# Kernel optimization log

Hardware: AMD Instinct MI355X
Metric: run time of the kernel (lower is better)

Reference implementation:

```python
import jax, jax.numpy as jnp
import numpy as np

NI = 512
HEADS = 8
DH = NI // HEADS  # 64 = attn_chans
EPS = 1e-5

def _ln(x, g, b):
    mu = jnp.mean(x, axis=-1, keepdims=True)
    var = jnp.var(x, axis=-1, keepdims=True)
    return (x - mu) * jax.lax.rsqrt(var + EPS) * g + b

def setup_inputs() -> dict:
    key = jax.random.key(0)
    ks = jax.random.split(key, 5)
    n, c, h, w = 8, NI, 32, 32
    return {
        "x": jax.random.normal(ks[0], (n, c, h, w), jnp.float32),
        "query_x": jax.random.normal(ks[1], (n, c, h, w), jnp.float32),
        "q_ln_g": jnp.ones((c,), jnp.float32),
        "q_ln_b": jnp.zeros((c,), jnp.float32),
        "q_w": jax.random.normal(ks[2], (c, c), jnp.float32) / np.sqrt(c),
        "q_b": jnp.zeros((c,), jnp.float32),
        "kv_ln_g": jnp.ones((c,), jnp.float32),
        "kv_ln_b": jnp.zeros((c,), jnp.float32),
        "kv_w": jax.random.normal(ks[3], (c, 2 * c), jnp.float32) / np.sqrt(c),
        "kv_b": jnp.zeros((2 * c,), jnp.float32),
        "proj_w": jax.random.normal(ks[4], (c, c), jnp.float32) / np.sqrt(c),
        "proj_b": jnp.zeros((c,), jnp.float32),
    }

def reference(x, query_x, q_ln_g, q_ln_b, q_w, q_b, kv_ln_g, kv_ln_b, kv_w, kv_b, proj_w, proj_b):
    n, c, h, w = x.shape
    s = h * w
    xs = x.reshape(n, c, s).transpose(0, 2, 1)        # (n, s, c)
    qx = query_x.reshape(n, c, s).transpose(0, 2, 1)  # (n, s, c)
    q_proj = _ln(qx, q_ln_g, q_ln_b) @ q_w + q_b        # (n, s, c)
    kv = _ln(xs, kv_ln_g, kv_ln_b) @ kv_w + kv_b        # (n, s, 2c)
    cat = jnp.concatenate([q_proj, kv], axis=-1)        # (n, s, 3c)
    # rearrange 'n s (h d3)' with h=HEADS, d3 = 3*DH, then chunk into q,k,v
    cat = cat.reshape(n, s, HEADS, 3 * DH).transpose(0, 2, 1, 3)  # (n, H, s, 3d)
    q, k, v = jnp.split(cat, 3, axis=-1)                # each (n, H, s, d)
    scale = jnp.sqrt(jnp.asarray(DH, q.dtype))          # sqrt(ni/nheads)
    scores = jnp.einsum('nhqd,nhkd->nhqk', q, k) / scale
    attn = jax.nn.softmax(scores, axis=-1)
    o = jnp.einsum('nhqk,nhkd->nhqd', attn, v)          # (n, H, s, d)
    o = o.transpose(0, 2, 1, 3).reshape(n, s, c)        # (n, s, c)
    o = o @ proj_w + proj_b
    return o.transpose(0, 2, 1).reshape(n, c, h, w)
```

## Files before the change

### kernel.cpp

```cpp
#include <hip/hip_runtime.h>
#include <math.h>

namespace {

constexpr int S = 1024;
constexpr int C = 512;
constexpr int NBATCH = 8;
constexpr int RTOT = NBATCH * S;
constexpr int HEADS = 8;
constexpr int DH = 64;

typedef __attribute__((ext_vector_type(8))) short bf16x8;
typedef __attribute__((ext_vector_type(4))) float f32x4;
typedef __attribute__((ext_vector_type(16))) float f32x16;
typedef unsigned short u16;
typedef unsigned int u32;

__device__ __forceinline__ u16 f2bf(float x) {
  union { float f; u32 u; } v; v.f = x;
  u32 r = v.u + 0x7FFF + ((v.u >> 16) & 1);
  return (u16)(r >> 16);
}
__device__ __forceinline__ float bf2f(u16 b) {
  union { u32 u; float f; } v; v.u = (u32)b << 16; return v.f;
}
__device__ __forceinline__ u32 cvtpk(float a, float b) {
  u32 r;
  asm("v_cvt_pk_bf16_f32 %0, %1, %2" : "=v"(r) : "v"(a), "v"(b));
  return r;
}
__device__ __forceinline__ float fexp2(float x) {
  float r;
  asm("v_exp_f32 %0, %1" : "=v"(r) : "v"(x));
  return r;
}
__device__ __forceinline__ void gl_lds16(const void* g, void* l) {
  auto gp = (const __attribute__((address_space(1))) u32*)g;
  auto lp = (__attribute__((address_space(3))) u32*)l;
  __builtin_amdgcn_global_load_lds(gp, lp, 16, 0, 0);
}

__global__ void ln_fused(const float* __restrict__ x, const float* __restrict__ qx,
                         const float* __restrict__ gx, const float* __restrict__ bx,
                         const float* __restrict__ gq, const float* __restrict__ bq,
                         u16* __restrict__ Xkv, u16* __restrict__ Xq) {
  __shared__ float Ssum[8][32], Ssq[8][32];
  __shared__ float mu_s[32], rs_s[32];
  __shared__ float T[32][65];
  int t = threadIdx.x;
  int si0 = blockIdx.x * 32;
  int isq = blockIdx.y & 1, n = blockIdx.y >> 1;
  const float* in = isq ? qx : x;
  const float* g  = isq ? gq : gx;
  const float* be = isq ? bq : bx;
  u16* out = isq ? Xq : Xkv;

  {
    int sl = t & 31, cg = t >> 5;
    const float* p = in + ((size_t)n * C + cg * 64) * S + si0 + sl;
    float s = 0.f, sq = 0.f;
#pragma unroll 8
    for (int c = 0; c < 64; c++) { float v = p[(size_t)c * S]; s += v; sq += v * v; }
    Ssum[cg][sl] = s; Ssq[cg][sl] = sq;
  }
  __syncthreads();
  if (t < 32) {
    float ss = 0.f, q2 = 0.f;
#pragma unroll
    for (int i = 0; i < 8; i++) { ss += Ssum[i][t]; q2 += Ssq[i][t]; }
    float m = ss * (1.0f / C);
    float var = q2 * (1.0f / C) - m * m;
    mu_s[t] = m; rs_s[t] = rsqrtf(var + 1e-5f);
  }
  __syncthreads();

  int si4 = (t & 7) * 4, cl = t >> 3;
  float4 mu4 = *(const float4*)&mu_s[si4];
  float4 rs4 = *(const float4*)&rs_s[si4];
  int wsl = t >> 3, wc8 = (t & 7) * 8;

  for (int c0 = 0; c0 < C; c0 += 64) {
#pragma unroll
    for (int i = 0; i < 2; i++) {
      int c = c0 + cl + i * 32;
      float4 v = *(const float4*)&in[((size_t)n * C + c) * S + si0 + si4];
      float gg = g[c], bb = be[c];
      T[si4 + 0][cl + i * 32] = (v.x - mu4.x) * rs4.x * gg + bb;
      T[si4 + 1][cl + i * 32] = (v.y - mu4.y) * rs4.y * gg + bb;
      T[si4 + 2][cl + i * 32] = (v.z - mu4.z) * rs4.z * gg + bb;
      T[si4 + 3][cl + i * 32] = (v.w - mu4.w) * rs4.w * gg + bb;
    }
    __syncthreads();
    u16 pk[8];
#pragma unroll
    for (int j = 0; j < 8; j++) pk[j] = f2bf(T[wsl][wc8 + j]);
    *(uint4*)&out[((size_t)(n * S + si0 + wsl)) * C + c0 + wc8] = *(const uint4*)pk;
    __syncthreads();
  }
}

__global__ void prep_w(const float* __restrict__ qw, const float* __restrict__ kvw,
                       const float* __restrict__ pw,
                       u16* __restrict__ Wtq, u16* __restrict__ Wtkv,
                       u16* __restrict__ Wph) {
  int z = blockIdx.z;
  int N = (z == 1) ? 1024 : 512;
  int col0 = blockIdx.y * 64;
  if (col0 >= N) return;
  int k0 = blockIdx.x * 64;
  const float* W = (z == 0) ? qw : (z == 1) ? kvw : pw;
  __shared__ float T[64][65];
  int t = threadIdx.x;
  int kl = t >> 4, c4 = (t & 15) * 4;
#pragma unroll
  for (int i = 0; i < 4; i++) {
    float4 v = *(const float4*)&W[(size_t)(k0 + kl + i * 16) * N + col0 + c4];
    T[kl + i * 16][c4 + 0] = v.x; T[kl + i * 16][c4 + 1] = v.y;
    T[kl + i * 16][c4 + 2] = v.z; T[kl + i * 16][c4 + 3] = v.w;
  }
  __syncthreads();
#pragma unroll
  for (int p = 0; p < 2; p++) {
    int cl = (t >> 3) + p * 32, k8 = (t & 7) * 8;
    u16 hi[8];
#pragma unroll
    for (int j = 0; j < 8; j++) hi[j] = f2bf(T[k8 + j][cl]);
    size_t o = (size_t)(col0 + cl) * 512 + k0 + k8;
    if (z == 0) *(uint4*)&Wtq[o] = *(const uint4*)hi;
    else if (z == 1) *(uint4*)&Wtkv[o] = *(const uint4*)hi;
    else *(uint4*)&Wph[o] = *(const uint4*)hi;
  }
}

__global__ __launch_bounds__(256, 4) void gemm_qkv(
    const u16* __restrict__ Xq, const u16* __restrict__ Xkv,
    const u16* __restrict__ Wtq, const u16* __restrict__ Wtkv,
    const float* __restrict__ q_b, const float* __restrict__ kv_b,
    u16* __restrict__ Qb, u16* __restrict__ Kb, u16* __restrict__ Vt) {
  __shared__ __attribute__((aligned(16))) u16 As[128 * 64];
  __shared__ __attribute__((aligned(16))) u16 Bs[128 * 64];
  int t = threadIdx.x, wid = t >> 6, lane = t & 63, lr = lane & 15, lg = lane >> 4;
  int colb = blockIdx.x;
  const u16* A; const u16* Wt; const float* bias; int ch0;
  if (colb < 4) { A = Xq;  Wt = Wtq  + (size_t)colb * 128 * 512;       bias = q_b  + colb * 128;       ch0 = colb * 128; }
  else          { A = Xkv; Wt = Wtkv + (size_t)(colb - 4) * 128 * 512; bias = kv_b + (colb - 4) * 128; ch0 = 512 + (colb - 4) * 128; }
  int row0 = blockIdx.y * 128;
  int wr = wid >> 1, wc = wid & 1;
  f32x4 acc[4][4];
#pragma unroll
  for (int m = 0; m < 4; m++)
#pragma unroll
    for (int n = 0; n < 4; n++) acc[m][n] = (f32x4){0.f, 0.f, 0.f, 0.f};

  for (int k0 = 0; k0 < 512; k0 += 64) {
    __syncthreads();
#pragma unroll
    for (int it = 0; it < 4; it++) {
      int chunk = (wid * 4 + it) * 64 + lane;
      int r = chunk >> 3, sg = chunk & 7;
      gl_lds16(A + (size_t)(row0 + r) * 512 + k0 + ((sg ^ (r & 7)) * 8),
               (char*)As + (size_t)chunk * 16);
    }
#pragma unroll
    for (int it = 0; it < 4; it++) {
      int chunk = (wid * 4 + it) * 64 + lane;
      int r = chunk >> 3, sg = chunk & 7;
      gl_lds16(Wt + (size_t)r * 512 + k0 + ((sg ^ (r & 7)) * 8),
               (char*)Bs + (size_t)chunk * 16);
    }
    __syncthreads();
#pragma unroll
    for (int kk = 0; kk < 2; kk++) {
      bf16x8 bfr[4];
#pragma unroll
      for (int n = 0; n < 4; n++) {
        int col = wc * 64 + n * 16 + lr;
        bfr[n] = *(const bf16x8*)((const char*)Bs + col * 128 + (((kk * 4 + lg) ^ (col & 7)) << 4));
      }
#pragma unroll
      for (int m = 0; m < 4; m++) {
        int row = wr * 64 + m * 16 + lr;
        bf16x8 af = *(const bf16x8*)((const char*)As + row * 128 + (((kk * 4 + lg) ^ (row & 7)) << 4));
#pragma unroll
        for (int n = 0; n < 4; n++)
          acc[m][n] = __builtin_amdgcn_mfma_f32_16x16x32_bf16(af, bfr[n], acc[m][n], 0, 0, 0);
      }
    }
  }
#pragma unroll
  for (int m = 0; m < 4; m++)
#pragma unroll
    for (int n = 0; n < 4; n++) {
      int colg = wc * 64 + n * 16 + lr;
      int ch = ch0 + colg;
      int h = ch / 192, role = (ch >> 6) % 3, d = ch & 63;
      float bs = bias[colg];
      float qsc = (role == 0) ? 0.18033688f : 1.0f;
      int growb = row0 + wr * 64 + m * 16 + lg * 4;
      int nn = growb >> 10, ssi0 = growb & (S - 1);
      size_t nh = (size_t)(nn * HEADS + h);
      if (role == 2) {
        u16 pk[4];
#pragma unroll
        for (int r = 0; r < 4; r++) pk[r] = f2bf(acc[m][n][r] + bs);
        *(uint2*)&Vt[(nh * DH + d) * S + ssi0] = *(const uint2*)pk;
      } else {
        u16* dst = (role == 0) ? Qb : Kb;
#pragma unroll
        for (int r = 0; r < 4; r++)
          dst[(nh * S + ssi0 + r) * DH + d] = f2bf((acc[m][n][r] + bs) * qsc);
      }
    }
}

__global__ __launch_bounds__(256) void gemm_proj(
    const u16* __restrict__ Aob, const u16* __restrict__ Wh,
    const float* __restrict__ bias, float* __restrict__ out) {
  __shared__ __attribute__((aligned(16))) u16 As[128 * 64];
  __shared__ __attribute__((aligned(16))) u16 Bh[64 * 64];
  int t = threadIdx.x, wid = t >> 6, lane = t & 63, lr = lane & 15, lg = lane >> 4;
  int ch0 = blockIdx.x * 64, row0 = blockIdx.y * 128;
  int wc = wid & 1, wr = wid >> 1;
  f32x4 acc[2][4];
#pragma unroll
  for (int m = 0; m < 2; m++)
#pragma unroll
    for (int n = 0; n < 4; n++) acc[m][n] = (f32x4){0.f, 0.f, 0.f, 0.f};

  for (int k0 = 0; k0 < 512; k0 += 64) {
    __syncthreads();
#pragma unroll
    for (int it = 0; it < 4; it++) {
      int idx = (wid * 4 + it) * 64 + lane;
      int r = idx >> 3, sg = idx & 7;
      gl_lds16(Aob + (size_t)(row0 + r) * 512 + k0 + ((sg ^ (r & 7)) * 8),
               (char*)As + (wid * 4 + it) * 1024);
    }
#pragma unroll
    for (int it = 0; it < 2; it++) {
      int idx = (wid * 2 + it) * 64 + lane;
      int r = idx >> 3, sg = idx & 7;
      gl_lds16(Wh + (size_t)(ch0 + r) * 512 + k0 + ((sg ^ (r & 7)) * 8),
               (char*)Bh + (wid * 2 + it) * 1024);
    }
    __syncthreads();
#pragma unroll
    for (int kk = 0; kk < 2; kk++) {
      bf16x8 ar[4];
#pragma unroll
      for (int n = 0; n < 4; n++) {
        int row = wr * 64 + n * 16 + lr;
        ar[n] = *(const bf16x8*)((const char*)As + row * 128 + (((kk * 4 + lg) ^ (row & 7)) << 4));
      }
#pragma unroll
      for (int m = 0; m < 2; m++) {
        int ch = wc * 32 + m * 16 + lr;
        bf16x8 bh = *(const bf16x8*)((const char*)Bh + ch * 128 + (((kk * 4 + lg) ^ (ch & 7)) << 4));
#pragma unroll
        for (int n = 0; n < 4; n++)
          acc[m][n] = __builtin_amdgcn_mfma_f32_16x16x32_bf16(bh, ar[n], acc[m][n], 0, 0, 0);
      }
    }
  }
#pragma unroll
  for (int m = 0; m < 2; m++)
#pragma unroll
    for (int n = 0; n < 4; n++) {
      int rowg = row0 + wr * 64 + n * 16 + lr;
      int nn = rowg >> 10, ssi = rowg & (S - 1);
#pragma unroll
      for (int r = 0; r < 4; r++) {
        int ch = ch0 + wc * 32 + m * 16 + lg * 4 + r;
        out[((size_t)nn * C + ch) * S + ssi] = acc[m][n][r] + bias[ch];
      }
    }
}

constexpr int KVB = 64;

__global__ __launch_bounds__(256, 4) void attn_kernel(
    const u16* __restrict__ Qbf, const u16* __restrict__ Kbf,
    const u16* __restrict__ Vtb, u16* __restrict__ Obf) {
  __shared__ __attribute__((aligned(16))) u16 Ks[2][KVB * DH];
  __shared__ __attribute__((aligned(16))) u16 Vs[2][DH * KVB];

  int tid = threadIdx.x;
  int wave = tid >> 6, lane = tid & 63;
  int lq = lane & 31, hi = lane >> 5;
  int qg = wave & 1, kg = wave >> 1;
  int w = (blockIdx.x & 7) * 128 + (blockIdx.x >> 3);
  int qt = w & 15, nh = w >> 4;
  const u16* Qg = Qbf + (size_t)nh * S * DH;
  const u16* Kg = Kbf + (size_t)nh * S * DH;
  const u16* Vg = Vtb + (size_t)nh * DH * S;

  int qrow = qt * 64 + qg * 32 + lq;
  bf16x8 qf[4];
#pragma unroll
  for (int ks = 0; ks < 4; ks++)
    qf[ks] = *(const bf16x8*)(Qg + (size_t)qrow * DH + ks * 16 + hi * 8);

  f32x16 oa0 = {}, oa1 = {};
  float m_run = -1e30f, l_run = 0.f;

  int e0i = tid, e1i = tid + 256;
  int r0 = e0i >> 3, sg0 = e0i & 7, r1 = e1i >> 3, sg1 = e1i & 7;
  char* kd0 = (char*)&Ks[0][0] + (e0i & ~63) * 16;
  char* kd1 = (char*)&Ks[0][0] + (e1i & ~63) * 16;
  char* vd0 = (char*)&Vs[0][0] + (e0i & ~63) * 16;
  char* vd1 = (char*)&Vs[0][0] + (e1i & ~63) * 16;

#define STAGE(kb, b)                                                             \
  do {                                                                           \
    gl_lds16(Kg + (size_t)((kb) * KVB + r0) * 64 + ((sg0 ^ (r0 & 7)) * 8),       \
             kd0 + (b) * (KVB * DH * 2));                                        \
    gl_lds16(Kg + (size_t)((kb) * KVB + r1) * 64 + ((sg1 ^ (r1 & 7)) * 8),       \
             kd1 + (b) * (KVB * DH * 2));                                        \
    gl_lds16(Vg + (size_t)r0 * S + (kb) * KVB + ((sg0 ^ (r0 & 7)) * 8),          \
             vd0 + (b) * (KVB * DH * 2));                                        \
    gl_lds16(Vg + (size_t)r1 * S + (kb) * KVB + ((sg1 ^ (r1 & 7)) * 8),          \
             vd1 + (b) * (KVB * DH * 2));                                        \
  } while (0)

  STAGE(0, 0);

  for (int kb = 0; kb < S / KVB; kb++) {
    int cur = kb & 1;
    __syncthreads();
    if (kb + 1 < S / KVB) STAGE(kb + 1, cur ^ 1);

    const char* Kc = (const char*)&Ks[cur][0];
    const char* Vc = (const char*)&Vs[cur][0];

    f32x16 sc = {};
#pragma unroll
    for (int ks = 0; ks < 4; ks++) {
      int sg = ks * 2 + hi;
      bf16x8 kf = *(const bf16x8*)(Kc + (kg * 32 + lq) * 128 + ((sg ^ (lq & 7)) << 4));
      sc = __builtin_amdgcn_mfma_f32_32x32x16_bf16(kf, qf[ks], sc, 0, 0, 0);
    }

    bf16x8 vfr[2][2];
#pragma unroll
    for (int kk = 0; kk < 2; kk++) {
      int sg = kg * 4 + kk * 2 + hi;
      vfr[kk][0] = *(const bf16x8*)(Vc + lq * 128 + ((sg ^ (lq & 7)) << 4));
      vfr[kk][1] = *(const bf16x8*)(Vc + (32 + lq) * 128 + ((sg ^ (lq & 7)) << 4));
    }

    float mx[8];
#pragma unroll
    for (int r = 0; r < 8; r++) mx[r] = fmaxf(sc[2 * r], sc[2 * r + 1]);
#pragma unroll
    for (int r = 0; r < 4; r++) mx[r] = fmaxf(mx[r], mx[r + 4]);
    float pmax = fmaxf(fmaxf(mx[0], mx[1]), fmaxf(mx[2], mx[3]));
    pmax = fmaxf(pmax, __shfl_xor(pmax, 32));

    if (!__all(pmax <= m_run + 11.5f)) {
      float mnew = fmaxf(m_run, pmax);
      float corr = fexp2(m_run - mnew);
      m_run = mnew;
      l_run *= corr;
#pragma unroll
      for (int r = 0; r < 16; r++) { oa0[r] *= corr; oa1[r] *= corr; }
    }

#pragma unroll
    for (int r = 0; r < 16; r++) sc[r] = fexp2(sc[r] - m_run);
    {
      float s8[8];
#pragma unroll
      for (int r = 0; r < 8; r++) s8[r] = sc[2 * r] + sc[2 * r + 1];
#pragma unroll
      for (int r = 0; r < 4; r++) s8[r] += s8[r + 4];
      float psum = (s8[0] + s8[1]) + (s8[2] + s8[3]);
      psum += __shfl_xor(psum, 32);
      l_run += psum;
    }

    u32 c[8];
    c[0] = cvtpk(sc[0],  sc[1]);  c[1] = cvtpk(sc[2],  sc[3]);
    c[2] = cvtpk(sc[4],  sc[5]);  c[3] = cvtpk(sc[6],  sc[7]);
    c[4] = cvtpk(sc[8],  sc[9]);  c[5] = cvtpk(sc[10], sc[11]);
    c[6] = cvtpk(sc[12], sc[13]); c[7] = cvtpk(sc[14], sc[15]);
    asm("v_permlane32_swap_b32 %0, %1" : "+v"(c[0]), "+v"(c[2]));
    asm("v_permlane32_swap_b32 %0, %1" : "+v"(c[1]), "+v"(c[3]));
    asm("v_permlane32_swap_b32 %0, %1" : "+v"(c[4]), "+v"(c[6]));
    asm("v_permlane32_swap_b32 %0, %1" : "+v"(c[5]), "+v"(c[7]));

#pragma unroll
    for (int kk = 0; kk < 2; kk++) {
      union { u32 u[4]; bf16x8 v; } pu;
      pu.u[0] = c[kk * 4 + 0]; pu.u[1] = c[kk * 4 + 1];
      pu.u[2] = c[kk * 4 + 2]; pu.u[3] = c[kk * 4 + 3];
      oa0 = __builtin_amdgcn_mfma_f32_32x32x16_bf16(vfr[kk][0], pu.v, oa0, 0, 0, 0);
      oa1 = __builtin_amdgcn_mfma_f32_32x32x16_bf16(vfr[kk][1], pu.v, oa1, 0, 0, 0);
    }
  }
#undef STAGE

  __syncthreads();
  float* exO = (float*)&Ks[0][0];
  float* exS = (float*)&Vs[0][0];
  if (kg) {
    float* o = exO + qg * 2048;
#pragma unroll
    for (int r = 0; r < 16; r++) {
      o[r * 64 + lane] = oa0[r];
      o[(16 + r) * 64 + lane] = oa1[r];
    }
    exS[qg * 128 + lane] = m_run;
    exS[qg * 128 + 64 + lane] = l_run;
  }
  __syncthreads();
  if (!kg) {
    float* o = exO + qg * 2048;
    float m2 = exS[qg * 128 + lane];
    float l2 = exS[qg * 128 + 64 + lane];
    float m = fmaxf(m_run, m2);
    float f0 = fexp2(m_run - m), f2 = fexp2(m2 - m);
    l_run = l_run * f0 + l2 * f2;
#pragma unroll
    for (int r = 0; r < 16; r++) {
      oa0[r] = oa0[r] * f0 + o[r * 64 + lane] * f2;
      oa1[r] = oa1[r] * f0 + o[(16 + r) * 64 + lane] * f2;
    }
    int n = nh >> 3, h = nh & 7;
    float lf = 1.0f / l_run;
    u16* orow = Obf + ((size_t)n * S + qrow) * C + h * DH;
#pragma unroll
    for (int rq = 0; rq < 4; rq++) {
      int d0 = rq * 8 + 4 * hi;
      uint2 w0, w1;
      w0.x = cvtpk(oa0[rq * 4 + 0] * lf, oa0[rq * 4 + 1] * lf);
      w0.y = cvtpk(oa0[rq * 4 + 2] * lf, oa0[rq * 4 + 3] * lf);
      w1.x = cvtpk(oa1[rq * 4 + 0] * lf, oa1[rq * 4 + 1] * lf);
      w1.y = cvtpk(oa1[rq * 4 + 2] * lf, oa1[rq * 4 + 3] * lf);
      *(uint2*)(orow + d0) = w0;
      *(uint2*)(orow + 32 + d0) = w1;
    }
  }
}

}

extern "C" void kernel_launch(void* const* d_in, const int* in_sizes, int n_in,
                              void* d_out, int out_size, void* d_ws, size_t ws_size,
                              hipStream_t stream) {
  const float* x       = (const float*)d_in[0];
  const float* qx      = (const float*)d_in[1];
  const float* q_ln_g  = (const float*)d_in[2];
  const float* q_ln_b  = (const float*)d_in[3];
  const float* q_w     = (const float*)d_in[4];
  const float* q_b     = (const float*)d_in[5];
  const float* kv_ln_g = (const float*)d_in[6];
  const float* kv_ln_b = (const float*)d_in[7];
  const float* kv_w    = (const float*)d_in[8];
  const float* kv_b    = (const float*)d_in[9];
  const float* proj_w  = (const float*)d_in[10];
  const float* proj_b  = (const float*)d_in[11];
  float* out = (float*)d_out;

  u16* u = (u16*)d_ws;
  u16* Xkv  = u;                u += (size_t)RTOT * C;
  u16* Xq   = u;                u += (size_t)RTOT * C;
  u16* Wtq  = u;                u += (size_t)C * C;
  u16* Wtkv = u;                u += (size_t)2 * C * C;
  u16* Wph  = u;                u += (size_t)C * C;
  u16* Qb   = u;                u += (size_t)NBATCH * HEADS * S * DH;
  u16* Kb   = u;                u += (size_t)NBATCH * HEADS * S * DH;
  u16* Vt   = u;                u += (size_t)NBATCH * HEADS * S * DH;
  u16* Obf  = u;

  hipLaunchKernelGGL(ln_fused, dim3(S / 32, 2 * NBATCH), dim3(256), 0, stream,
                     x, qx, kv_ln_g, kv_ln_b, q_ln_g, q_ln_b, Xkv, Xq);
  hipLaunchKernelGGL(prep_w, dim3(8, 16, 3), dim3(256), 0, stream,
                     q_w, kv_w, proj_w, Wtq, Wtkv, Wph);
  hipLaunchKernelGGL(gemm_qkv, dim3(12, RTOT / 128), dim3(256), 0, stream,
                     Xq, Xkv, Wtq, Wtkv, q_b, kv_b, Qb, Kb, Vt);
  hipLaunchKernelGGL(attn_kernel, dim3(1024), dim3(256), 0, stream,
                     Qb, Kb, Vt, Obf);
  hipLaunchKernelGGL(gemm_proj, dim3(C / 64, RTOT / 128), dim3(256), 0, stream,
                     Obf, Wph, proj_b, out);
}
```

Before: 88.11 us.

## Compute softmax row sums via MFMA, double-buffer LN transpose, tune proj occupancy

In attention, the per-row softmax denominator is now produced by an extra MFMA against a ones vector instead of a VALU reduction plus cross-lane shuffle, and the max reduction uses three-input max chains. The LayerNorm kernel double-buffers its LDS transpose tile so one of the two barriers per iteration can be dropped. gemm_proj gets a minimum-occupancy launch bound. The extra MFMA adds matrix-core work per tile, and the row sums are now accumulated from bf16-rounded probabilities rather than fp32 values.

```diff
diff --git a/kernel.cpp b/kernel.cpp
--- a/kernel.cpp
+++ b/kernel.cpp
@@ -34,6 +34,9 @@
   asm("v_exp_f32 %0, %1" : "=v"(r) : "v"(x));
   return r;
 }
+__device__ __forceinline__ float fmax3(float a, float b, float c) {
+  return fmaxf(fmaxf(a, b), c);
+}
 __device__ __forceinline__ void gl_lds16(const void* g, void* l) {
   auto gp = (const __attribute__((address_space(1))) u32*)g;
   auto lp = (__attribute__((address_space(3))) u32*)l;
@@ -46,7 +49,7 @@
                          u16* __restrict__ Xkv, u16* __restrict__ Xq) {
   __shared__ float Ssum[8][32], Ssq[8][32];
   __shared__ float mu_s[32], rs_s[32];
-  __shared__ float T[32][65];
+  __shared__ float T[2][32][65];
   int t = threadIdx.x;
   int si0 = blockIdx.x * 32;
   int isq = blockIdx.y & 1, n = blockIdx.y >> 1;
@@ -79,23 +82,23 @@
   float4 rs4 = *(const float4*)&rs_s[si4];
   int wsl = t >> 3, wc8 = (t & 7) * 8;
 
-  for (int c0 = 0; c0 < C; c0 += 64) {
+  for (int it = 0; it < 8; it++) {
+    int c0 = it * 64, b = it & 1;
 #pragma unroll
     for (int i = 0; i < 2; i++) {
       int c = c0 + cl + i * 32;
       float4 v = *(const float4*)&in[((size_t)n * C + c) * S + si0 + si4];
       float gg = g[c], bb = be[c];
-      T[si4 + 0][cl + i * 32] = (v.x - mu4.x) * rs4.x * gg + bb;
-      T[si4 + 1][cl + i * 32] = (v.y - mu4.y) * rs4.y * gg + bb;
-      T[si4 + 2][cl + i * 32] = (v.z - mu4.z) * rs4.z * gg + bb;
-      T[si4 + 3][cl + i * 32] = (v.w - mu4.w) * rs4.w * gg + bb;
+      T[b][si4 + 0][cl + i * 32] = (v.x - mu4.x) * rs4.x * gg + bb;
+      T[b][si4 + 1][cl + i * 32] = (v.y - mu4.y) * rs4.y * gg + bb;
+      T[b][si4 + 2][cl + i * 32] = (v.z - mu4.z) * rs4.z * gg + bb;
+      T[b][si4 + 3][cl + i * 32] = (v.w - mu4.w) * rs4.w * gg + bb;
     }
     __syncthreads();
     u16 pk[8];
 #pragma unroll
-    for (int j = 0; j < 8; j++) pk[j] = f2bf(T[wsl][wc8 + j]);
+    for (int j = 0; j < 8; j++) pk[j] = f2bf(T[b][wsl][wc8 + j]);
     *(uint4*)&out[((size_t)(n * S + si0 + wsl)) * C + c0 + wc8] = *(const uint4*)pk;
-    __syncthreads();
   }
 }
 
@@ -213,7 +216,7 @@
     }
 }
 
-__global__ __launch_bounds__(256) void gemm_proj(
+__global__ __launch_bounds__(256, 4) void gemm_proj(
     const u16* __restrict__ Aob, const u16* __restrict__ Wh,
     const float* __restrict__ bias, float* __restrict__ out) {
   __shared__ __attribute__((aligned(16))) u16 As[128 * 64];
@@ -300,8 +303,12 @@
   for (int ks = 0; ks < 4; ks++)
     qf[ks] = *(const bf16x8*)(Qg + (size_t)qrow * DH + ks * 16 + hi * 8);
 
-  f32x16 oa0 = {}, oa1 = {};
-  float m_run = -1e30f, l_run = 0.f;
+  bf16x8 ones;
+#pragma unroll
+  for (int i = 0; i < 8; i++) ones[i] = (short)0x3F80;
+
+  f32x16 oa0 = {}, oa1 = {}, lacc = {};
+  float m_run = -1e30f;
 
   int e0i = tid, e1i = tid + 256;
   int r0 = e0i >> 3, sg0 = e0i & 7, r1 = e1i >> 3, sg1 = e1i & 7;
@@ -348,35 +355,25 @@
       vfr[kk][1] = *(const bf16x8*)(Vc + (32 + lq) * 128 + ((sg ^ (lq & 7)) << 4));
     }
 
-    float mx[8];
-#pragma unroll
-    for (int r = 0; r < 8; r++) mx[r] = fmaxf(sc[2 * r], sc[2 * r + 1]);
-#pragma unroll
-    for (int r = 0; r < 4; r++) mx[r] = fmaxf(mx[r], mx[r + 4]);
-    float pmax = fmaxf(fmaxf(mx[0], mx[1]), fmaxf(mx[2], mx[3]));
+    float g0 = fmax3(sc[0], sc[1], sc[2]);
+    float g1 = fmax3(sc[3], sc[4], sc[5]);
+    float g2 = fmax3(sc[6], sc[7], sc[8]);
+    float g3 = fmax3(sc[9], sc[10], sc[11]);
+    float g4 = fmax3(sc[12], sc[13], sc[14]);
+    float pmax = fmax3(fmax3(g0, g1, g2), fmaxf(g3, g4), sc[15]);
     pmax = fmaxf(pmax, __shfl_xor(pmax, 32));
 
     if (!__all(pmax <= m_run + 11.5f)) {
       float mnew = fmaxf(m_run, pmax);
       float corr = fexp2(m_run - mnew);
       m_run = mnew;
-      l_run *= corr;
+      lacc[0] *= corr;
 #pragma unroll
       for (int r = 0; r < 16; r++) { oa0[r] *= corr; oa1[r] *= corr; }
     }
 
 #pragma unroll
     for (int r = 0; r < 16; r++) sc[r] = fexp2(sc[r] - m_run);
-    {
-      float s8[8];
-#pragma unroll
-      for (int r = 0; r < 8; r++) s8[r] = sc[2 * r] + sc[2 * r + 1];
-#pragma unroll
-      for (int r = 0; r < 4; r++) s8[r] += s8[r + 4];
-      float psum = (s8[0] + s8[1]) + (s8[2] + s8[3]);
-      psum += __shfl_xor(psum, 32);
-      l_run += psum;
-    }
 
     u32 c[8];
     c[0] = cvtpk(sc[0],  sc[1]);  c[1] = cvtpk(sc[2],  sc[3]);
@@ -393,12 +390,14 @@
       union { u32 u[4]; bf16x8 v; } pu;
       pu.u[0] = c[kk * 4 + 0]; pu.u[1] = c[kk * 4 + 1];
       pu.u[2] = c[kk * 4 + 2]; pu.u[3] = c[kk * 4 + 3];
+      lacc = __builtin_amdgcn_mfma_f32_32x32x16_bf16(ones, pu.v, lacc, 0, 0, 0);
       oa0 = __builtin_amdgcn_mfma_f32_32x32x16_bf16(vfr[kk][0], pu.v, oa0, 0, 0, 0);
       oa1 = __builtin_amdgcn_mfma_f32_32x32x16_bf16(vfr[kk][1], pu.v, oa1, 0, 0, 0);
     }
   }
 #undef STAGE
 
+  float l_run = lacc[0];
   __syncthreads();
   float* exO = (float*)&Ks[0][0];
   float* exS = (float*)&Vs[0][0];
```

New measurement: 87.06 us. Within noise of the previous version (-1.2%).
